# Kernel tuning notes

Measured on AMD Instinct MI355X. Metric: run time of the kernel, lower is better.

Reference implementation:

```python
import jax, jax.numpy as jnp
import numpy as np

N_NODES = 100000

def gcn_conv(x, src, dst, W, b, n):
    # PyG GCNConv: h = W x; add self-loops; norm = d^-1/2[src] * d^-1/2[dst]; scatter-add at dst; + b
    h = x @ W
    loop = jnp.arange(n, dtype=src.dtype)
    s = jnp.concatenate([src, loop])
    d = jnp.concatenate([dst, loop])
    deg = jax.ops.segment_sum(jnp.ones_like(d, dtype=h.dtype), d, num_segments=n)
    dis = jnp.where(deg > 0, jax.lax.rsqrt(deg), 0.0)
    norm = dis[s] * dis[d]                     # [E+n]
    msg = h[s] * norm[:, None]                  # [E+n, F] big gather
    out = jax.ops.segment_sum(msg, d, num_segments=n)
    return out + b

def setup_inputs() -> dict:
    key = jax.random.key(0)
    ks = jax.random.split(key, 12)
    n, e, f = N_NODES, 3200000, 14
    hid = [64, 64, 32]
    c = 2
    x = jax.random.normal(ks[0], (n, f), dtype=jnp.float32)
    edge_index = jax.random.randint(ks[1], (2, e), 0, n, dtype=jnp.int64)
    batch = jnp.sort(jax.random.randint(ks[2], (n,), 0, 2000, dtype=jnp.int64))
    def lin(k, fi, fo):
        s = 1.0 / np.sqrt(fi)
        return jax.random.uniform(k, (fi, fo), jnp.float32, -s, s)
    W1 = lin(ks[3], f, hid[0]); b1 = jnp.zeros((hid[0],), jnp.float32)
    W2 = lin(ks[4], hid[0], hid[1]); b2 = jnp.zeros((hid[1],), jnp.float32)
    W3 = lin(ks[5], hid[1], hid[2]); b3 = jnp.zeros((hid[2],), jnp.float32)
    W4 = lin(ks[6], hid[2], c); b4 = jnp.zeros((c,), jnp.float32)
    return {"x": x, "edge_index": edge_index, "batch": batch, "num_graphs": 2000,
            "W1": W1, "b1": b1, "W2": W2, "b2": b2, "W3": W3, "b3": b3, "W4": W4, "b4": b4}

def reference(x, edge_index, batch, num_graphs, W1, b1, W2, b2, W3, b3, W4, b4):
    n = x.shape[0]
    src, dst = edge_index[0], edge_index[1]
    h = jax.nn.relu(gcn_conv(x, src, dst, W1, b1, n))   # dropout = identity at inference
    h = jax.nn.relu(gcn_conv(h, src, dst, W2, b2, n))
    h = jax.nn.relu(gcn_conv(h, src, dst, W3, b3, n))
    h = gcn_conv(h, src, dst, W4, b4, n)
    # global mean pool over graphs
    sums = jax.ops.segment_sum(h, batch, num_segments=num_graphs)
    cnts = jax.ops.segment_sum(jnp.ones((n,), h.dtype), batch, num_segments=num_graphs)
    pooled = sums / jnp.maximum(cnts, 1.0)[:, None]
    return jax.nn.log_softmax(pooled, axis=-1)
```

## Files before the change

kernel.cpp:

```cpp
#include <hip/hip_runtime.h>
#include <hip/hip_fp16.h>
#include <math.h>
#include <type_traits>

static constexpr int THREADS = 256;
static constexpr int CAP   = 80;
static constexpr int BSH   = 10;
static constexpr int SUBS  = 8;
static constexpr int SUBN  = 128;
static constexpr int CAPB  = 34816;
static constexpr int MAXB  = 128;


__global__ void k_zero_i(int* __restrict__ p, int n) {
    int i = blockIdx.x * blockDim.x + threadIdx.x;
    if (i < n) p[i] = 0;
}


__global__ __launch_bounds__(THREADS)
void k_part(const int* __restrict__ src, const int* __restrict__ dst,
            int* __restrict__ bcnt, int* __restrict__ pairs, int e, int nbuck) {
    __shared__ int hist[MAXB];
    __shared__ int base_s[MAXB];
    for (int i = threadIdx.x; i < nbuck; i += THREADS) hist[i] = 0;
    __syncthreads();

    int i0 = (blockIdx.x * THREADS + (int)threadIdx.x) * 8;
    int ss[8], dd[8], bb[8], rk[8];
    int c8 = 0;
    if (i0 < e) {
        c8 = min(8, e - i0);
        if (c8 == 8) {
            int4 d0 = ((const int4*)(dst + i0))[0];
            int4 d1 = ((const int4*)(dst + i0))[1];
            int4 s0 = ((const int4*)(src + i0))[0];
            int4 s1 = ((const int4*)(src + i0))[1];
            dd[0]=d0.x; dd[1]=d0.y; dd[2]=d0.z; dd[3]=d0.w;
            dd[4]=d1.x; dd[5]=d1.y; dd[6]=d1.z; dd[7]=d1.w;
            ss[0]=s0.x; ss[1]=s0.y; ss[2]=s0.z; ss[3]=s0.w;
            ss[4]=s1.x; ss[5]=s1.y; ss[6]=s1.z; ss[7]=s1.w;
        } else {
            for (int j = 0; j < c8; ++j) { dd[j] = dst[i0 + j]; ss[j] = src[i0 + j]; }
        }
        for (int j = 0; j < c8; ++j) {
            bb[j] = dd[j] >> BSH;
            rk[j] = atomicAdd(&hist[bb[j]], 1);
        }
    }
    __syncthreads();
    for (int i = threadIdx.x; i < nbuck; i += THREADS)
        base_s[i] = hist[i] ? atomicAdd(&bcnt[i], hist[i]) : 0;
    __syncthreads();
    for (int j = 0; j < c8; ++j) {
        int idx = base_s[bb[j]] + rk[j];
        if (idx < CAPB)
            pairs[(size_t)bb[j] * CAPB + idx] = ((dd[j] & ((1 << BSH) - 1)) << 17) | ss[j];
    }
}


__global__ __launch_bounds__(THREADS)
void k_scat2(const int* __restrict__ pairs, const int* __restrict__ bcnt,
             int* __restrict__ cnt, int* __restrict__ csr, int n) {
    __shared__ int slab[SUBN * CAP];
    __shared__ int lcnt[SUBN];
    int bucket = blockIdx.x / SUBS;
    int sub    = blockIdx.x % SUBS;
    int gnode0 = (bucket << BSH) + sub * SUBN;
    if (gnode0 >= n) return;
    for (int i = threadIdx.x; i < SUBN; i += THREADS) lcnt[i] = 0;
    __syncthreads();

    int m = min(bcnt[bucket], CAPB);
    const int* pp = pairs + (size_t)bucket * CAPB;
    for (int i0 = (int)threadIdx.x * 4; i0 < m; i0 += THREADS * 4) {
        int k = min(4, m - i0);
        int v[4];
        if (k == 4) {
            int4 a = *(const int4*)(pp + i0);
            v[0] = a.x; v[1] = a.y; v[2] = a.z; v[3] = a.w;
        } else {
            for (int j = 0; j < k; ++j) v[j] = pp[i0 + j];
        }
#pragma unroll
        for (int j = 0; j < 4; ++j) {
            if (j < k) {
                int dl = v[j] >> 17;
                if ((dl >> 7) == sub) {
                    int ln = dl & (SUBN - 1);
                    int p = atomicAdd(&lcnt[ln], 1);
                    if (p < CAP) slab[ln * CAP + p] = v[j] & 0x1FFFF;
                }
            }
        }
    }
    __syncthreads();

    size_t gbase = (size_t)gnode0 * CAP;
    for (int idx = threadIdx.x; idx < SUBN * CAP; idx += THREADS) {
        int node = gnode0 + idx / CAP;
        if (node < n) csr[gbase + idx] = slab[idx];
    }
    for (int i = threadIdx.x; i < SUBN; i += THREADS) {
        int node = gnode0 + i;
        if (node < n) cnt[node] = min(lcnt[i], CAP);
    }
}


__global__ __launch_bounds__(THREADS)
void k_dis_xs(const int* __restrict__ deg, const float* __restrict__ x,
              float* __restrict__ dis, __half2* __restrict__ xs, int n) {
    int i = blockIdx.x * blockDim.x + threadIdx.x;
    if (i >= n) return;
    float dn = rsqrtf((float)(deg[i] + 1));
    dis[i] = dn;
    const float* xr = x + (size_t)i * 14;
    __half2* o = xs + (size_t)i * 8;
#pragma unroll
    for (int fl = 0; fl < 7; ++fl) {
        float2 v;
        v.x = dn * xr[fl * 2];
        v.y = dn * xr[fl * 2 + 1];
        o[fl] = __float22half2_rn(v);
    }
    o[7] = __float22half2_rn(make_float2(0.f, 0.f));
}


template<int SG, int HPL, bool SELF_SCALE, bool EPI_SCALE, bool BIAS, bool RELU>
__global__ __launch_bounds__(THREADS)
void k_gather_pk(const __half2* __restrict__ hw, const int* __restrict__ deg,
                 const int* __restrict__ csr, const float* __restrict__ dis,
                 const float* __restrict__ bias, float* __restrict__ out, int n) {
    constexpr int RS = SG * HPL;
    int tid = blockIdx.x * THREADS + threadIdx.x;
    int node = tid / SG;
    int fl = tid % SG;
    if (node >= n) return;
    size_t o = (size_t)node * CAP;
    int dg = deg[node];
    float dn = dis[node];

    auto loadrow = [&](int s, __half2* r) {
        const __half2* p = hw + (size_t)s * RS + fl * HPL;
        if constexpr (HPL == 4) {
            union { uint4 u; __half2 h[4]; } t;
            t.u = *(const uint4*)p;
            r[0] = t.h[0]; r[1] = t.h[1]; r[2] = t.h[2]; r[3] = t.h[3];
        } else if constexpr (HPL == 2) {
            union { uint2 u; __half2 h[2]; } t;
            t.u = *(const uint2*)p;
            r[0] = t.h[0]; r[1] = t.h[1];
        } else {
            r[0] = *p;
        }
    };

    float2 self[HPL];
    {
        __half2 r[HPL];
        loadrow(node, r);
#pragma unroll
        for (int q = 0; q < HPL; ++q) {
            self[q] = __half22float2(r[q]);
            if (SELF_SCALE) { self[q].x *= dn; self[q].y *= dn; }
        }
    }

    __half2 z = __float2half2_rn(0.f);
    __half2 c0[HPL], c1[HPL], c2[HPL], c3[HPL];
#pragma unroll
    for (int q = 0; q < HPL; ++q) { c0[q] = z; c1[q] = z; c2[q] = z; c3[q] = z; }

    int base = 0;
    for (; base + SG <= dg; base += SG) {
        int cs = csr[o + base + fl];
#pragma unroll
        for (int t = 0; t < SG; t += 4) {
            int s0 = __shfl(cs, t, SG),     s1 = __shfl(cs, t + 1, SG);
            int s2 = __shfl(cs, t + 2, SG), s3 = __shfl(cs, t + 3, SG);
            __half2 r0[HPL], r1[HPL], r2[HPL], r3[HPL];
            loadrow(s0, r0); loadrow(s1, r1); loadrow(s2, r2); loadrow(s3, r3);
#pragma unroll
            for (int q = 0; q < HPL; ++q) {
                c0[q] = __hadd2(c0[q], r0[q]);
                c1[q] = __hadd2(c1[q], r1[q]);
                c2[q] = __hadd2(c2[q], r2[q]);
                c3[q] = __hadd2(c3[q], r3[q]);
            }
        }
    }
    int rem = dg - base;
    if (rem > 0) {
        int cs = (fl < rem) ? csr[o + base + fl] : 0;
        int t = 0;
        for (; t + 4 <= rem; t += 4) {
            int s0 = __shfl(cs, t, SG),     s1 = __shfl(cs, t + 1, SG);
            int s2 = __shfl(cs, t + 2, SG), s3 = __shfl(cs, t + 3, SG);
            __half2 r0[HPL], r1[HPL], r2[HPL], r3[HPL];
            loadrow(s0, r0); loadrow(s1, r1); loadrow(s2, r2); loadrow(s3, r3);
#pragma unroll
            for (int q = 0; q < HPL; ++q) {
                c0[q] = __hadd2(c0[q], r0[q]);
                c1[q] = __hadd2(c1[q], r1[q]);
                c2[q] = __hadd2(c2[q], r2[q]);
                c3[q] = __hadd2(c3[q], r3[q]);
            }
        }
        for (; t < rem; ++t) {
            int s = __shfl(cs, t, SG);
            __half2 r[HPL];
            loadrow(s, r);
#pragma unroll
            for (int q = 0; q < HPL; ++q) c0[q] = __hadd2(c0[q], r[q]);
        }
    }

    float* op = out + (size_t)node * 2 * RS + fl * 2 * HPL;
#pragma unroll
    for (int q = 0; q < HPL; ++q) {
        float2 v0 = __half22float2(c0[q]), v1 = __half22float2(c1[q]);
        float2 v2 = __half22float2(c2[q]), v3 = __half22float2(c3[q]);
        float2 v;
        v.x = self[q].x + (v0.x + v1.x) + (v2.x + v3.x);
        v.y = self[q].y + (v0.y + v1.y) + (v2.y + v3.y);
        if (EPI_SCALE) { v.x *= dn; v.y *= dn; }
        if (BIAS) {
            float2 b = ((const float2*)bias)[fl * HPL + q];
            v.x += b.x; v.y += b.y;
        }
        if (RELU) { v.x = fmaxf(v.x, 0.f); v.y = fmaxf(v.y, 0.f); }
        op[q * 2 + 0] = v.x;
        op[q * 2 + 1] = v.y;
    }
}

__global__ __launch_bounds__(THREADS)
void k_gather2(const float* __restrict__ hw, const int* __restrict__ deg,
               const int* __restrict__ csr, const float* __restrict__ dis,
               const float* __restrict__ b, float* __restrict__ out, int n) {
    int i = blockIdx.x * blockDim.x + threadIdx.x;
    if (i >= n) return;
    const float2* h2 = (const float2*)hw;
    size_t o = (size_t)i * CAP;
    int dg = deg[i];
    float2 a = h2[i];
    float x0 = a.x, y0 = a.y, x1 = 0.f, y1 = 0.f, x2 = 0.f, y2 = 0.f, x3 = 0.f, y3 = 0.f;
    int j = 0;
    for (; j + 4 <= dg; j += 4) {
        int s0 = csr[o + j], s1 = csr[o + j + 1], s2 = csr[o + j + 2], s3 = csr[o + j + 3];
        float2 v0 = h2[s0], v1 = h2[s1], v2 = h2[s2], v3 = h2[s3];
        x0 += v0.x; y0 += v0.y;
        x1 += v1.x; y1 += v1.y;
        x2 += v2.x; y2 += v2.y;
        x3 += v3.x; y3 += v3.y;
    }
    for (; j < dg; ++j) {
        int s = csr[o + j];
        float2 v = h2[s];
        x0 += v.x; y0 += v.y;
    }
    float dn = dis[i];
    out[(size_t)i * 2 + 0] = ((x0 + x1) + (x2 + x3)) * dn + b[0];
    out[(size_t)i * 2 + 1] = ((y0 + y1) + (y2 + y3)) * dn + b[1];
}


template<int KW, int K, int KSTR, int FOUT, bool EPI_BIAS_RELU, typename OUT_T>
__global__ __launch_bounds__(THREADS)
void k_gemm_rb(const float* __restrict__ in, const float* __restrict__ W,
               const float* __restrict__ dis, const float* __restrict__ bias,
               OUT_T* __restrict__ out, int n) {
    constexpr int CG = FOUT / 4;
    __shared__ float Ws[K * FOUT];
    for (int i = threadIdx.x; i < K * FOUT; i += THREADS) {
        int r = i / FOUT;
        Ws[i] = (r < KW) ? W[i] : 0.0f;
    }
    __syncthreads();
    int gid = blockIdx.x * THREADS + threadIdx.x;
    int pair = gid / CG, cg = gid % CG;
    int node0 = pair * 2;
    if (node0 >= n) return;
    bool two = (node0 + 1 < n);
    const float4* r0 = (const float4*)(in + (size_t)node0 * KSTR);
    const float4* r1 = two ? (const float4*)(in + (size_t)(node0 + 1) * KSTR) : r0;
    const float4* Wf4 = (const float4*)Ws;
    float4 acc0 = {0.f, 0.f, 0.f, 0.f}, acc1 = {0.f, 0.f, 0.f, 0.f};
#pragma unroll
    for (int k0 = 0; k0 < K / 4; ++k0) {
        float4 x0 = r0[k0];
        float4 x1 = r1[k0];
#pragma unroll
        for (int kk = 0; kk < 4; ++kk) {
            float4 wv = Wf4[(k0 * 4 + kk) * CG + cg];
            float a = (&x0.x)[kk], b = (&x1.x)[kk];
            acc0.x += a * wv.x; acc0.y += a * wv.y; acc0.z += a * wv.z; acc0.w += a * wv.w;
            acc1.x += b * wv.x; acc1.y += b * wv.y; acc1.z += b * wv.z; acc1.w += b * wv.w;
        }
    }
    float dn0 = dis[node0];
    float dn1 = two ? dis[node0 + 1] : 0.f;
    acc0.x *= dn0; acc0.y *= dn0; acc0.z *= dn0; acc0.w *= dn0;
    acc1.x *= dn1; acc1.y *= dn1; acc1.z *= dn1; acc1.w *= dn1;
    if (EPI_BIAS_RELU) {
        float4 bv = ((const float4*)bias)[cg];
        acc0.x = fmaxf(acc0.x + bv.x, 0.f); acc0.y = fmaxf(acc0.y + bv.y, 0.f);
        acc0.z = fmaxf(acc0.z + bv.z, 0.f); acc0.w = fmaxf(acc0.w + bv.w, 0.f);
        acc1.x = fmaxf(acc1.x + bv.x, 0.f); acc1.y = fmaxf(acc1.y + bv.y, 0.f);
        acc1.z = fmaxf(acc1.z + bv.z, 0.f); acc1.w = fmaxf(acc1.w + bv.w, 0.f);
    }
    if constexpr (std::is_same<OUT_T, __half>::value) {
        union { __half2 h[2]; uint2 u; } p0, p1;
        p0.h[0] = __floats2half2_rn(acc0.x, acc0.y);
        p0.h[1] = __floats2half2_rn(acc0.z, acc0.w);
        *(uint2*)(out + (size_t)node0 * FOUT + cg * 4) = p0.u;
        if (two) {
            p1.h[0] = __floats2half2_rn(acc1.x, acc1.y);
            p1.h[1] = __floats2half2_rn(acc1.z, acc1.w);
            *(uint2*)(out + (size_t)(node0 + 1) * FOUT + cg * 4) = p1.u;
        }
    } else {
        ((float4*)(out + (size_t)node0 * FOUT))[cg] = acc0;
        if (two) ((float4*)(out + (size_t)(node0 + 1) * FOUT))[cg] = acc1;
    }
}

template<int KSTR, int K, int FOUT>
__global__ __launch_bounds__(THREADS)
void k_gemm_sm(const float* __restrict__ in, const float* __restrict__ W,
               const float* __restrict__ dis, float* __restrict__ out, int n) {
    __shared__ float Ws[K * FOUT];
    for (int i = threadIdx.x; i < K * FOUT; i += THREADS) Ws[i] = W[i];
    __syncthreads();
    int gid = blockIdx.x * THREADS + threadIdx.x;
    int node = gid / FOUT, col = gid % FOUT;
    if (node >= n) return;
    const float* xr = in + (size_t)node * KSTR;
    float acc = 0.0f;
#pragma unroll
    for (int k = 0; k < K; ++k) acc += xr[k] * Ws[k * FOUT + col];
    out[(size_t)node * FOUT + col] = acc * dis[node];
}


__global__ void k_zero2(float* __restrict__ sums, float* __restrict__ cnts, int ng) {
    int i = blockIdx.x * blockDim.x + threadIdx.x;
    if (i < ng) {
        sums[i * 2 + 0] = 0.0f;
        sums[i * 2 + 1] = 0.0f;
        cnts[i] = 0.0f;
    }
}

__global__ __launch_bounds__(THREADS)
void k_pool(const float* __restrict__ h4, const int* __restrict__ batch,
            float* __restrict__ sums, float* __restrict__ cnts, int n) {
    int i0 = (blockIdx.x * blockDim.x + threadIdx.x) * 8;
    if (i0 >= n) return;
    int end = min(i0 + 8, n);
    int g = batch[i0];
    float v0 = 0.f, v1 = 0.f, c = 0.f;
    for (int i = i0; i < end; ++i) {
        int gi = batch[i];
        if (gi != g) {
            atomicAdd(&sums[g * 2 + 0], v0);
            atomicAdd(&sums[g * 2 + 1], v1);
            atomicAdd(&cnts[g], c);
            g = gi; v0 = 0.f; v1 = 0.f; c = 0.f;
        }
        v0 += h4[(size_t)i * 2 + 0];
        v1 += h4[(size_t)i * 2 + 1];
        c += 1.0f;
    }
    atomicAdd(&sums[g * 2 + 0], v0);
    atomicAdd(&sums[g * 2 + 1], v1);
    atomicAdd(&cnts[g], c);
}

__global__ void k_logsoftmax(const float* __restrict__ sums, const float* __restrict__ cnts,
                             float* __restrict__ out, int ng) {
    int g = blockIdx.x * blockDim.x + threadIdx.x;
    if (g >= ng) return;
    float c = fmaxf(cnts[g], 1.0f);
    float p0 = sums[g * 2 + 0] / c;
    float p1 = sums[g * 2 + 1] / c;
    float m = fmaxf(p0, p1);
    float l = m + logf(expf(p0 - m) + expf(p1 - m));
    out[g * 2 + 0] = p0 - l;
    out[g * 2 + 1] = p1 - l;
}


static inline int nblk(long long t) { return (int)((t + THREADS - 1) / THREADS); }

extern "C" void kernel_launch(void* const* d_in, const int* in_sizes, int n_in,
                              void* d_out, int out_size, void* d_ws, size_t ws_size,
                              hipStream_t stream) {
    const float* x     = (const float*)d_in[0];
    const int*   ei    = (const int*)d_in[1];
    const int*   batch = (const int*)d_in[2];
    const float* W1 = (const float*)d_in[4];
    const float* b1 = (const float*)d_in[5];
    const float* W2 = (const float*)d_in[6];
    const float* b2 = (const float*)d_in[7];
    const float* W3 = (const float*)d_in[8];
    const float* b3 = (const float*)d_in[9];
    const float* W4 = (const float*)d_in[10];
    const float* b4 = (const float*)d_in[11];

    const int n  = in_sizes[0] / 14;
    const int e  = in_sizes[1] / 2;
    const int ng = out_size / 2;
    const int* src = ei;
    const int* dst = ei + e;
    const int nb = nblk(n);
    const int nbuck = (n + (1 << BSH) - 1) >> BSH;

    char* ws = (char*)d_ws;
    size_t off_b = 0;
    auto alloc = [&](size_t bytes) -> char* {
        char* p = ws + off_b;
        off_b = (off_b + bytes + 255) & ~(size_t)255;
        return p;
    };
    int*     cnt  = (int*)alloc((size_t)n * 4);
    int*     bcnt = (int*)alloc((size_t)MAXB * 4);
    float*   dis  = (float*)alloc((size_t)n * 4);
    int*     csr  = (int*)alloc((size_t)n * CAP * 4);
    __half2* xs16 = (__half2*)alloc((size_t)n * 8 * 4);
    float*   agg1 = (float*)alloc((size_t)n * 16 * 4);
    float*   hbuf = (float*)alloc((size_t)n * 64 * 4);
    __half2* hw16 = (__half2*)alloc((size_t)n * 32 * 4);
    float*   hw4  = (float*)alloc((size_t)n * 2 * 4);
    float*   h4   = (float*)alloc((size_t)n * 2 * 4);
    float*   sums = (float*)alloc((size_t)ng * 2 * 4);
    float*   cnts = (float*)alloc((size_t)ng * 4);
    int*     pairs = (int*)hbuf;
    (void)ws_size; (void)n_in;

    k_zero_i<<<1, THREADS, 0, stream>>>(bcnt, MAXB);
    k_part<<<nblk(((long long)e + 7) / 8), THREADS, 0, stream>>>(src, dst, bcnt, pairs, e, nbuck);
    k_scat2<<<nbuck * SUBS, THREADS, 0, stream>>>(pairs, bcnt, cnt, csr, n);
    k_dis_xs<<<nb, THREADS, 0, stream>>>(cnt, x, dis, xs16, n);

    k_gather_pk<4, 2, true, false, false, false><<<nblk((long long)n * 4), THREADS, 0, stream>>>(
        xs16, cnt, csr, dis, nullptr, agg1, n);
    k_gemm_rb<14, 16, 16, 64, true, float><<<nblk((long long)(n / 2 + 1) * 16), THREADS, 0, stream>>>(
        agg1, W1, dis, b1, hbuf, n);

    k_gemm_rb<64, 64, 64, 64, false, __half><<<nblk((long long)(n / 2 + 1) * 16), THREADS, 0, stream>>>(
        hbuf, W2, dis, nullptr, (__half*)hw16, n);
    k_gather_pk<8, 4, false, true, true, true><<<nblk((long long)n * 8), THREADS, 0, stream>>>(
        hw16, cnt, csr, dis, b2, hbuf, n);

    k_gemm_rb<64, 64, 64, 32, false, __half><<<nblk((long long)(n / 2 + 1) * 8), THREADS, 0, stream>>>(
        hbuf, W3, dis, nullptr, (__half*)hw16, n);
    k_gather_pk<4, 4, false, true, true, true><<<nblk((long long)n * 4), THREADS, 0, stream>>>(
        hw16, cnt, csr, dis, b3, hbuf, n);

    k_gemm_sm<32, 32, 2><<<nblk((long long)n * 2), THREADS, 0, stream>>>(
        hbuf, W4, dis, hw4, n);
    k_gather2<<<nb, THREADS, 0, stream>>>(hw4, cnt, csr, dis, b4, h4, n);

    k_zero2<<<nblk(ng), THREADS, 0, stream>>>(sums, cnts, ng);
    k_pool<<<nblk((n + 7) / 8), THREADS, 0, stream>>>(h4, batch, sums, cnts, n);
    k_logsoftmax<<<nblk(ng), THREADS, 0, stream>>>(sums, cnts, (float*)d_out, ng);
}
```

Baseline: 351.8 us.

## Fuse layer-3 gather with layer-4 GEMM, fuse final gather with pooling, retune partition

The layer-3 aggregation kernel now applies bias and ReLU and multiplies by W4 in registers, reducing across a 4-lane subgroup with shuffles. This removes the separate small GEMM and the 32-wide intermediate write and read. The last gather atomically adds each node's result straight into the per-graph sums, which removes the h4 buffer and the pool kernel but issues one atomic per node instead of one per run of nodes. The GEMM kernels now compute four nodes per thread instead of two, and the edge-partition bucket sizes are halved (more buckets, fewer sub-blocks).

```diff
diff --git a/kernel.cpp b/kernel.cpp
--- a/kernel.cpp
+++ b/kernel.cpp
@@ -5,11 +5,11 @@
 
 static constexpr int THREADS = 256;
 static constexpr int CAP   = 80;
-static constexpr int BSH   = 10;
-static constexpr int SUBS  = 8;
+static constexpr int BSH   = 9;
+static constexpr int SUBS  = 4;
 static constexpr int SUBN  = 128;
-static constexpr int CAPB  = 34816;
-static constexpr int MAXB  = 128;
+static constexpr int CAPB  = 17920;
+static constexpr int MAXB  = 256;
 
 
 __global__ void k_zero_i(int* __restrict__ p, int n) {
@@ -237,42 +237,135 @@
     }
 }
 
-__global__ __launch_bounds__(THREADS)
-void k_gather2(const float* __restrict__ hw, const int* __restrict__ deg,
-               const int* __restrict__ csr, const float* __restrict__ dis,
-               const float* __restrict__ b, float* __restrict__ out, int n) {
+
+__global__ __launch_bounds__(THREADS)
+void k_gather_l3(const __half2* __restrict__ hw, const int* __restrict__ deg,
+                 const int* __restrict__ csr, const float* __restrict__ dis,
+                 const float* __restrict__ b3, const float* __restrict__ W4,
+                 float2* __restrict__ hw4, int n) {
+    constexpr int SG = 4, HPL = 4, RS = 16;
+    __shared__ float Ws4[64];
+    if (threadIdx.x < 64) Ws4[threadIdx.x] = W4[threadIdx.x];
+    __syncthreads();
+
+    int tid = blockIdx.x * THREADS + threadIdx.x;
+    int node = tid / SG;
+    int fl = tid % SG;
+    if (node >= n) return;
+    size_t o = (size_t)node * CAP;
+    int dg = deg[node];
+    float dn = dis[node];
+
+    auto loadrow = [&](int s, __half2* r) {
+        union { uint4 u; __half2 h[4]; } t;
+        t.u = *(const uint4*)(hw + (size_t)s * RS + fl * HPL);
+        r[0] = t.h[0]; r[1] = t.h[1]; r[2] = t.h[2]; r[3] = t.h[3];
+    };
+
+    float2 self[HPL];
+    {
+        __half2 r[HPL];
+        loadrow(node, r);
+#pragma unroll
+        for (int q = 0; q < HPL; ++q) self[q] = __half22float2(r[q]);
+    }
+
+    __half2 z = __float2half2_rn(0.f);
+    __half2 c0[HPL], c1[HPL], c2[HPL], c3[HPL];
+#pragma unroll
+    for (int q = 0; q < HPL; ++q) { c0[q] = z; c1[q] = z; c2[q] = z; c3[q] = z; }
+
+    int base = 0;
+    for (; base + SG <= dg; base += SG) {
+        int cs = csr[o + base + fl];
+#pragma unroll
+        for (int t = 0; t < SG; t += 4) {
+            int s0 = __shfl(cs, t, SG),     s1 = __shfl(cs, t + 1, SG);
+            int s2 = __shfl(cs, t + 2, SG), s3 = __shfl(cs, t + 3, SG);
+            __half2 r0[HPL], r1[HPL], r2[HPL], r3[HPL];
+            loadrow(s0, r0); loadrow(s1, r1); loadrow(s2, r2); loadrow(s3, r3);
+#pragma unroll
+            for (int q = 0; q < HPL; ++q) {
+                c0[q] = __hadd2(c0[q], r0[q]);
+                c1[q] = __hadd2(c1[q], r1[q]);
+                c2[q] = __hadd2(c2[q], r2[q]);
+                c3[q] = __hadd2(c3[q], r3[q]);
+            }
+        }
+    }
+    int rem = dg - base;
+    if (rem > 0) {
+        int cs = (fl < rem) ? csr[o + base + fl] : 0;
+        for (int t = 0; t < rem; ++t) {
+            int s = __shfl(cs, t, SG);
+            __half2 r[HPL];
+            loadrow(s, r);
+#pragma unroll
+            for (int q = 0; q < HPL; ++q) c0[q] = __hadd2(c0[q], r[q]);
+        }
+    }
+
+    float p0 = 0.f, p1 = 0.f;
+#pragma unroll
+    for (int q = 0; q < HPL; ++q) {
+        float2 v0 = __half22float2(c0[q]), v1 = __half22float2(c1[q]);
+        float2 v2 = __half22float2(c2[q]), v3 = __half22float2(c3[q]);
+        float2 v;
+        v.x = self[q].x + (v0.x + v1.x) + (v2.x + v3.x);
+        v.y = self[q].y + (v0.y + v1.y) + (v2.y + v3.y);
+        v.x *= dn; v.y *= dn;
+        float2 b = ((const float2*)b3)[fl * HPL + q];
+        v.x = fmaxf(v.x + b.x, 0.f);
+        v.y = fmaxf(v.y + b.y, 0.f);
+        int f = 8 * fl + 2 * q;
+        p0 += v.x * Ws4[f * 2 + 0] + v.y * Ws4[(f + 1) * 2 + 0];
+        p1 += v.x * Ws4[f * 2 + 1] + v.y * Ws4[(f + 1) * 2 + 1];
+    }
+    p0 += __shfl_xor(p0, 1, SG); p0 += __shfl_xor(p0, 2, SG);
+    p1 += __shfl_xor(p1, 1, SG); p1 += __shfl_xor(p1, 2, SG);
+    if (fl == 0) hw4[node] = make_float2(p0 * dn, p1 * dn);
+}
+
+
+__global__ __launch_bounds__(THREADS)
+void k_gather2p(const float2* __restrict__ hw, const int* __restrict__ deg,
+                const int* __restrict__ csr, const float* __restrict__ dis,
+                const float* __restrict__ b, const int* __restrict__ batch,
+                float* __restrict__ sums, float* __restrict__ cnts, int n) {
     int i = blockIdx.x * blockDim.x + threadIdx.x;
     if (i >= n) return;
-    const float2* h2 = (const float2*)hw;
     size_t o = (size_t)i * CAP;
     int dg = deg[i];
-    float2 a = h2[i];
+    float2 a = hw[i];
     float x0 = a.x, y0 = a.y, x1 = 0.f, y1 = 0.f, x2 = 0.f, y2 = 0.f, x3 = 0.f, y3 = 0.f;
     int j = 0;
     for (; j + 4 <= dg; j += 4) {
         int s0 = csr[o + j], s1 = csr[o + j + 1], s2 = csr[o + j + 2], s3 = csr[o + j + 3];
-        float2 v0 = h2[s0], v1 = h2[s1], v2 = h2[s2], v3 = h2[s3];
+        float2 v0 = hw[s0], v1 = hw[s1], v2 = hw[s2], v3 = hw[s3];
         x0 += v0.x; y0 += v0.y;
         x1 += v1.x; y1 += v1.y;
         x2 += v2.x; y2 += v2.y;
         x3 += v3.x; y3 += v3.y;
     }
     for (; j < dg; ++j) {
-        int s = csr[o + j];
-        float2 v = h2[s];
+        float2 v = hw[csr[o + j]];
         x0 += v.x; y0 += v.y;
     }
     float dn = dis[i];
-    out[(size_t)i * 2 + 0] = ((x0 + x1) + (x2 + x3)) * dn + b[0];
-    out[(size_t)i * 2 + 1] = ((y0 + y1) + (y2 + y3)) * dn + b[1];
+    float h0 = ((x0 + x1) + (x2 + x3)) * dn + b[0];
+    float h1 = ((y0 + y1) + (y2 + y3)) * dn + b[1];
+    int g = batch[i];
+    atomicAdd(&sums[g * 2 + 0], h0);
+    atomicAdd(&sums[g * 2 + 1], h1);
+    atomicAdd(&cnts[g], 1.0f);
 }
 
 
 template<int KW, int K, int KSTR, int FOUT, bool EPI_BIAS_RELU, typename OUT_T>
 __global__ __launch_bounds__(THREADS)
-void k_gemm_rb(const float* __restrict__ in, const float* __restrict__ W,
-               const float* __restrict__ dis, const float* __restrict__ bias,
-               OUT_T* __restrict__ out, int n) {
+void k_gemm_rb4(const float* __restrict__ in, const float* __restrict__ W,
+                const float* __restrict__ dis, const float* __restrict__ bias,
+                OUT_T* __restrict__ out, int n) {
     constexpr int CG = FOUT / 4;
     __shared__ float Ws[K * FOUT];
     for (int i = threadIdx.x; i < K * FOUT; i += THREADS) {
@@ -281,68 +374,52 @@
     }
     __syncthreads();
     int gid = blockIdx.x * THREADS + threadIdx.x;
-    int pair = gid / CG, cg = gid % CG;
-    int node0 = pair * 2;
+    int quad = gid / CG, cg = gid % CG;
+    int node0 = quad * 4;
     if (node0 >= n) return;
-    bool two = (node0 + 1 < n);
-    const float4* r0 = (const float4*)(in + (size_t)node0 * KSTR);
-    const float4* r1 = two ? (const float4*)(in + (size_t)(node0 + 1) * KSTR) : r0;
+    int nn = min(4, n - node0);
+    const float* base = in + (size_t)node0 * KSTR;
     const float4* Wf4 = (const float4*)Ws;
-    float4 acc0 = {0.f, 0.f, 0.f, 0.f}, acc1 = {0.f, 0.f, 0.f, 0.f};
+    float4 acc[4];
+#pragma unroll
+    for (int j = 0; j < 4; ++j) acc[j] = make_float4(0.f, 0.f, 0.f, 0.f);
 #pragma unroll
     for (int k0 = 0; k0 < K / 4; ++k0) {
-        float4 x0 = r0[k0];
-        float4 x1 = r1[k0];
+        float4 xv[4];
+#pragma unroll
+        for (int j = 0; j < 4; ++j)
+            xv[j] = ((const float4*)(base + (size_t)(j < nn ? j : 0) * KSTR))[k0];
 #pragma unroll
         for (int kk = 0; kk < 4; ++kk) {
             float4 wv = Wf4[(k0 * 4 + kk) * CG + cg];
-            float a = (&x0.x)[kk], b = (&x1.x)[kk];
-            acc0.x += a * wv.x; acc0.y += a * wv.y; acc0.z += a * wv.z; acc0.w += a * wv.w;
-            acc1.x += b * wv.x; acc1.y += b * wv.y; acc1.z += b * wv.z; acc1.w += b * wv.w;
-        }
-    }
-    float dn0 = dis[node0];
-    float dn1 = two ? dis[node0 + 1] : 0.f;
-    acc0.x *= dn0; acc0.y *= dn0; acc0.z *= dn0; acc0.w *= dn0;
-    acc1.x *= dn1; acc1.y *= dn1; acc1.z *= dn1; acc1.w *= dn1;
-    if (EPI_BIAS_RELU) {
-        float4 bv = ((const float4*)bias)[cg];
-        acc0.x = fmaxf(acc0.x + bv.x, 0.f); acc0.y = fmaxf(acc0.y + bv.y, 0.f);
-        acc0.z = fmaxf(acc0.z + bv.z, 0.f); acc0.w = fmaxf(acc0.w + bv.w, 0.f);
-        acc1.x = fmaxf(acc1.x + bv.x, 0.f); acc1.y = fmaxf(acc1.y + bv.y, 0.f);
-        acc1.z = fmaxf(acc1.z + bv.z, 0.f); acc1.w = fmaxf(acc1.w + bv.w, 0.f);
-    }
-    if constexpr (std::is_same<OUT_T, __half>::value) {
-        union { __half2 h[2]; uint2 u; } p0, p1;
-        p0.h[0] = __floats2half2_rn(acc0.x, acc0.y);
-        p0.h[1] = __floats2half2_rn(acc0.z, acc0.w);
-        *(uint2*)(out + (size_t)node0 * FOUT + cg * 4) = p0.u;
-        if (two) {
-            p1.h[0] = __floats2half2_rn(acc1.x, acc1.y);
-            p1.h[1] = __floats2half2_rn(acc1.z, acc1.w);
-            *(uint2*)(out + (size_t)(node0 + 1) * FOUT + cg * 4) = p1.u;
-        }
-    } else {
-        ((float4*)(out + (size_t)node0 * FOUT))[cg] = acc0;
-        if (two) ((float4*)(out + (size_t)(node0 + 1) * FOUT))[cg] = acc1;
-    }
-}
-
-template<int KSTR, int K, int FOUT>
-__global__ __launch_bounds__(THREADS)
-void k_gemm_sm(const float* __restrict__ in, const float* __restrict__ W,
-               const float* __restrict__ dis, float* __restrict__ out, int n) {
-    __shared__ float Ws[K * FOUT];
-    for (int i = threadIdx.x; i < K * FOUT; i += THREADS) Ws[i] = W[i];
-    __syncthreads();
-    int gid = blockIdx.x * THREADS + threadIdx.x;
-    int node = gid / FOUT, col = gid % FOUT;
-    if (node >= n) return;
-    const float* xr = in + (size_t)node * KSTR;
-    float acc = 0.0f;
-#pragma unroll
-    for (int k = 0; k < K; ++k) acc += xr[k] * Ws[k * FOUT + col];
-    out[(size_t)node * FOUT + col] = acc * dis[node];
+#pragma unroll
+            for (int j = 0; j < 4; ++j) {
+                float a = (&xv[j].x)[kk];
+                acc[j].x += a * wv.x; acc[j].y += a * wv.y;
+                acc[j].z += a * wv.z; acc[j].w += a * wv.w;
+            }
+        }
+    }
+    float4 bv = EPI_BIAS_RELU ? ((const float4*)bias)[cg] : make_float4(0.f, 0.f, 0.f, 0.f);
+#pragma unroll
+    for (int j = 0; j < 4; ++j) {
+        if (j >= nn) break;
+        float dn = dis[node0 + j];
+        float4 v = acc[j];
+        v.x *= dn; v.y *= dn; v.z *= dn; v.w *= dn;
+        if (EPI_BIAS_RELU) {
+            v.x = fmaxf(v.x + bv.x, 0.f); v.y = fmaxf(v.y + bv.y, 0.f);
+            v.z = fmaxf(v.z + bv.z, 0.f); v.w = fmaxf(v.w + bv.w, 0.f);
+        }
+        if constexpr (std::is_same<OUT_T, __half>::value) {
+            union { __half2 h[2]; uint2 u; } p;
+            p.h[0] = __floats2half2_rn(v.x, v.y);
+            p.h[1] = __floats2half2_rn(v.z, v.w);
+            *(uint2*)(out + (size_t)(node0 + j) * FOUT + cg * 4) = p.u;
+        } else {
+            ((float4*)(out + (size_t)(node0 + j) * FOUT))[cg] = v;
+        }
+    }
 }
 
 
@@ -353,31 +430,6 @@
         sums[i * 2 + 1] = 0.0f;
         cnts[i] = 0.0f;
     }
-}
-
-__global__ __launch_bounds__(THREADS)
-void k_pool(const float* __restrict__ h4, const int* __restrict__ batch,
-            float* __restrict__ sums, float* __restrict__ cnts, int n) {
-    int i0 = (blockIdx.x * blockDim.x + threadIdx.x) * 8;
-    if (i0 >= n) return;
-    int end = min(i0 + 8, n);
-    int g = batch[i0];
-    float v0 = 0.f, v1 = 0.f, c = 0.f;
-    for (int i = i0; i < end; ++i) {
-        int gi = batch[i];
-        if (gi != g) {
-            atomicAdd(&sums[g * 2 + 0], v0);
-            atomicAdd(&sums[g * 2 + 1], v1);
-            atomicAdd(&cnts[g], c);
-            g = gi; v0 = 0.f; v1 = 0.f; c = 0.f;
-        }
-        v0 += h4[(size_t)i * 2 + 0];
-        v1 += h4[(size_t)i * 2 + 1];
-        c += 1.0f;
-    }
-    atomicAdd(&sums[g * 2 + 0], v0);
-    atomicAdd(&sums[g * 2 + 1], v1);
-    atomicAdd(&cnts[g], c);
 }
 
 __global__ void k_logsoftmax(const float* __restrict__ sums, const float* __restrict__ cnts,
@@ -435,7 +487,6 @@
     float*   hbuf = (float*)alloc((size_t)n * 64 * 4);
     __half2* hw16 = (__half2*)alloc((size_t)n * 32 * 4);
     float*   hw4  = (float*)alloc((size_t)n * 2 * 4);
-    float*   h4   = (float*)alloc((size_t)n * 2 * 4);
     float*   sums = (float*)alloc((size_t)ng * 2 * 4);
     float*   cnts = (float*)alloc((size_t)ng * 4);
     int*     pairs = (int*)hbuf;
@@ -448,24 +499,20 @@
 
     k_gather_pk<4, 2, true, false, false, false><<<nblk((long long)n * 4), THREADS, 0, stream>>>(
         xs16, cnt, csr, dis, nullptr, agg1, n);
-    k_gemm_rb<14, 16, 16, 64, true, float><<<nblk((long long)(n / 2 + 1) * 16), THREADS, 0, stream>>>(
+    k_gemm_rb4<14, 16, 16, 64, true, float><<<nblk((long long)((n + 3) / 4) * 16), THREADS, 0, stream>>>(
         agg1, W1, dis, b1, hbuf, n);
 
-    k_gemm_rb<64, 64, 64, 64, false, __half><<<nblk((long long)(n / 2 + 1) * 16), THREADS, 0, stream>>>(
+    k_gemm_rb4<64, 64, 64, 64, false, __half><<<nblk((long long)((n + 3) / 4) * 16), THREADS, 0, stream>>>(
         hbuf, W2, dis, nullptr, (__half*)hw16, n);
     k_gather_pk<8, 4, false, true, true, true><<<nblk((long long)n * 8), THREADS, 0, stream>>>(
         hw16, cnt, csr, dis, b2, hbuf, n);
 
-    k_gemm_rb<64, 64, 64, 32, false, __half><<<nblk((long long)(n / 2 + 1) * 8), THREADS, 0, stream>>>(
+    k_gemm_rb4<64, 64, 64, 32, false, __half><<<nblk((long long)((n + 3) / 4) * 8), THREADS, 0, stream>>>(
         hbuf, W3, dis, nullptr, (__half*)hw16, n);
-    k_gather_pk<4, 4, false, true, true, true><<<nblk((long long)n * 4), THREADS, 0, stream>>>(
-        hw16, cnt, csr, dis, b3, hbuf, n);
-
-    k_gemm_sm<32, 32, 2><<<nblk((long long)n * 2), THREADS, 0, stream>>>(
-        hbuf, W4, dis, hw4, n);
-    k_gather2<<<nb, THREADS, 0, stream>>>(hw4, cnt, csr, dis, b4, h4, n);
+    k_gather_l3<<<nblk((long long)n * 4), THREADS, 0, stream>>>(
+        hw16, cnt, csr, dis, b3, W4, (float2*)hw4, n);
 
     k_zero2<<<nblk(ng), THREADS, 0, stream>>>(sums, cnts, ng);
-    k_pool<<<nblk((n + 7) / 8), THREADS, 0, stream>>>(h4, batch, sums, cnts, n);
+    k_gather2p<<<nb, THREADS, 0, stream>>>((const float2*)hw4, cnt, csr, dis, b4, batch, sums, cnts, n);
     k_logsoftmax<<<nblk(ng), THREADS, 0, stream>>>(sums, cnts, (float*)d_out, ng);
 }
```

New measurement: 377.6 us. 7.3% more time.
